# Kernel optimization log

Measured on AMD Instinct MI355X. Metric: run time of the kernel, lower is better.

## Reference

```python
import jax, jax.numpy as jnp
import numpy as np

QMIN, QMAX = -128, 127

def make_accurate_lut():
    # lut[i, j] = signed8(j) * signed8(i) with indices taken as uint8 bit patterns
    v = np.arange(256)
    v[v >= 128] -= 256
    xx, yy = np.meshgrid(v, v)
    return jnp.asarray((xx * yy).astype(np.int32))

def setup_inputs() -> dict:
    key = jax.random.key(0)
    kx, kw = jax.random.split(key)
    B, N, M, K = 4, 512, 512, 256
    x = jax.random.normal(kx, (B, N, M), dtype=jnp.float32)
    w = jax.random.normal(kw, (K, M), dtype=jnp.float32)
    return {
        "x": x,
        "w": w,
        "lut": make_accurate_lut(),                       # [256,256] int32
        "x_scale": jnp.ones((1,), jnp.float32) * 0.03,    # per-tensor affine quant params
        "x_zero_point": jnp.zeros((1,), jnp.float32),
        "w_scale": jnp.ones((1,), jnp.float32) * 0.03,
        "w_zero_point": jnp.zeros((1,), jnp.float32),
    }

def _quantize(t, scale, zp):
    # affine quantize to signed int8 range, kept in int32 for indexing
    q = jnp.round(t / scale + zp)
    return jnp.clip(q, QMIN, QMAX).astype(jnp.int32)

def _lut_gemm(xq, wq, lut):
    # xq: [B,N,M] int32 in [-128,127]; wq: [K,M]; lut: [256,256]
    xi = jnp.mod(xq, 256)  # uint8 bit-pattern index
    wi = jnp.mod(wq, 256)
    # gather per-element products via the LUT, then accumulate over M
    prods = lut[xi[:, :, None, :], wi[None, None, :, :]]  # [B,N,K,M] int32
    return prods.sum(axis=-1)                             # [B,N,K] int32

def reference(x, w, lut, x_scale, x_zero_point, w_scale, w_zero_point):
    xs, xzp = x_scale.reshape(()), x_zero_point.reshape(())
    ws, wzp = w_scale.reshape(()), w_zero_point.reshape(())
    M = x.shape[-1]
    xq = _quantize(x, xs, xzp)           # [B,N,M]
    wq = _quantize(w, ws, wzp)           # [K,M]
    acc = _lut_gemm(xq, wq, lut).astype(jnp.float32)  # ~ sum_m xq*wq via LUT
    # affine zero-point correction: sum (xq-xzp)(wq-wzp)
    acc = (acc
           - wzp * jnp.sum(xq, axis=-1, keepdims=True).astype(jnp.float32)
           - xzp * jnp.sum(wq, axis=-1).astype(jnp.float32)[None, None, :]
           + jnp.float32(M) * xzp * wzp)
    return acc * xs * ws                 # dequantized output [B,N,K]
```

## Files before the change

### kernel.cpp

```cpp
#include <hip/hip_runtime.h>

constexpr int Mdim = 512;
constexpr int Kdim = 256;
constexpr int ROWS = 2048;

typedef int v4i __attribute__((ext_vector_type(4)));

__device__ __forceinline__ int qz(float v, float scale, float zp) {
    float q = rintf(v / scale + zp);
    q = fminf(fmaxf(q, -128.0f), 127.0f);
    return (int)q;
}

__device__ __forceinline__ int qp4(float4 f, float s, float zp) {
    int q0 = qz(f.x, s, zp), q1 = qz(f.y, s, zp);
    int q2 = qz(f.z, s, zp), q3 = qz(f.w, s, zp);
    return (q0 & 255) | ((q1 & 255) << 8) | ((q2 & 255) << 16) | ((q3 & 255) << 24);
}

__global__ __launch_bounds__(64) void fused_lutgemm_kernel(
        const float* __restrict__ x, const float* __restrict__ w,
        const float* __restrict__ x_scale, const float* __restrict__ x_zp,
        const float* __restrict__ w_scale, const float* __restrict__ w_zp,
        float* __restrict__ out) {
    const int lane  = threadIdx.x;
    const int group = lane >> 4;
    const int lo    = lane & 15;
    const int r0 = (blockIdx.x >> 3) * 16;
    const int c0 = (blockIdx.x & 7) * 32;

    const float xs   = x_scale[0], xzpf = x_zp[0];
    const float wsf  = w_scale[0], wzpf = w_zp[0];

    const float4* xr  = (const float4*)(x + (size_t)(r0 + lo) * Mdim) + group * 4;
    const float4* wr0 = (const float4*)(w + (size_t)(c0 + lo) * Mdim) + group * 4;
    const float4* wr1 = (const float4*)(w + (size_t)(c0 + 16 + lo) * Mdim) + group * 4;

    v4i a[8], b0[8], b1[8];
    #pragma unroll
    for (int kk = 0; kk < 8; ++kk) {
        float4 f0 = xr[kk * 16 + 0], f1 = xr[kk * 16 + 1];
        float4 f2 = xr[kk * 16 + 2], f3 = xr[kk * 16 + 3];
        float4 g0 = wr0[kk * 16 + 0], g1 = wr0[kk * 16 + 1];
        float4 g2 = wr0[kk * 16 + 2], g3 = wr0[kk * 16 + 3];
        float4 h0 = wr1[kk * 16 + 0], h1 = wr1[kk * 16 + 1];
        float4 h2 = wr1[kk * 16 + 2], h3 = wr1[kk * 16 + 3];
        a[kk]  = (v4i){ qp4(f0, xs, xzpf),  qp4(f1, xs, xzpf),
                        qp4(f2, xs, xzpf),  qp4(f3, xs, xzpf) };
        b0[kk] = (v4i){ qp4(g0, wsf, wzpf), qp4(g1, wsf, wzpf),
                        qp4(g2, wsf, wzpf), qp4(g3, wsf, wzpf) };
        b1[kk] = (v4i){ qp4(h0, wsf, wzpf), qp4(h1, wsf, wzpf),
                        qp4(h2, wsf, wzpf), qp4(h3, wsf, wzpf) };
    }

    const v4i ones = {0x01010101, 0x01010101, 0x01010101, 0x01010101};
    v4i acc0  = {0, 0, 0, 0};
    v4i acc1  = {0, 0, 0, 0};
    v4i accxs = {0, 0, 0, 0};
    v4i accw0 = {0, 0, 0, 0};
    v4i accw1 = {0, 0, 0, 0};
    #pragma unroll
    for (int kk = 0; kk < 8; ++kk) {
        acc0  = __builtin_amdgcn_mfma_i32_16x16x64_i8(a[kk], b0[kk], acc0, 0, 0, 0);
        acc1  = __builtin_amdgcn_mfma_i32_16x16x64_i8(a[kk], b1[kk], acc1, 0, 0, 0);
        accxs = __builtin_amdgcn_mfma_i32_16x16x64_i8(a[kk], ones,   accxs, 0, 0, 0);
        accw0 = __builtin_amdgcn_mfma_i32_16x16x64_i8(ones,  b0[kk], accw0, 0, 0, 0);
        accw1 = __builtin_amdgcn_mfma_i32_16x16x64_i8(ones,  b1[kk], accw1, 0, 0, 0);
    }

    const float oscale    = xs * wsf;
    const float base_corr = (float)Mdim * xzpf * wzpf;
    const float corr0 = base_corr - xzpf * (float)accw0[0];
    const float corr1 = base_corr - xzpf * (float)accw1[0];

    #pragma unroll
    for (int i = 0; i < 4; ++i) {
        const int row = r0 + group * 4 + i;
        const float xc = wzpf * (float)accxs[i];
        float v0 = (float)acc0[i] - xc + corr0;
        float v1 = (float)acc1[i] - xc + corr1;
        out[(size_t)row * Kdim + c0 + lo]      = v0 * oscale;
        out[(size_t)row * Kdim + c0 + 16 + lo] = v1 * oscale;
    }
}

extern "C" void kernel_launch(void* const* d_in, const int* in_sizes, int n_in,
                              void* d_out, int out_size, void* d_ws, size_t ws_size,
                              hipStream_t stream) {
    const float* x       = (const float*)d_in[0];
    const float* w       = (const float*)d_in[1];
    const float* x_scale = (const float*)d_in[3];
    const float* x_zp    = (const float*)d_in[4];
    const float* w_scale = (const float*)d_in[5];
    const float* w_zp    = (const float*)d_in[6];
    float* out = (float*)d_out;
    (void)d_ws; (void)ws_size;

    fused_lutgemm_kernel<<<(ROWS / 16) * (Kdim / 32), 64, 0, stream>>>(
        x, w, x_scale, x_zp, w_scale, w_zp, out);
}
```

Baseline: 82.11 us.

## Share quantized weight tile across four waves via swizzled LDS

Each block now covers 64 rows with four waves instead of one wave per 16-row tile. The 32x512 weight slice is quantized once per block into XOR-swizzled shared memory and read by all waves, so each block does a quarter of the previous redundant weight loads and quantization. This adds a block-wide barrier and 16KB of LDS per block, and cuts the number of blocks by four, which lowers available parallelism.

```diff
diff --git a/kernel.cpp b/kernel.cpp
--- a/kernel.cpp
+++ b/kernel.cpp
@@ -18,39 +18,59 @@
     return (q0 & 255) | ((q1 & 255) << 8) | ((q2 & 255) << 16) | ((q3 & 255) << 24);
 }
 
-__global__ __launch_bounds__(64) void fused_lutgemm_kernel(
+__global__ __launch_bounds__(256) void fused_lutgemm_kernel(
         const float* __restrict__ x, const float* __restrict__ w,
         const float* __restrict__ x_scale, const float* __restrict__ x_zp,
         const float* __restrict__ w_scale, const float* __restrict__ w_zp,
         float* __restrict__ out) {
-    const int lane  = threadIdx.x;
+    __shared__ int bq[32 * 128];
+
+    const int tid = threadIdx.x;
+    const int r0 = (blockIdx.x >> 3) * 64;
+    const int c0 = (blockIdx.x & 7) * 32;
+
+    const float xs  = x_scale[0], xzpf = x_zp[0];
+    const float wsf = w_scale[0], wzpf = w_zp[0];
+
+    {
+        const int br = tid >> 3;
+        const int g0 = (tid & 7) * 4;
+        const float4* src = (const float4*)(w + (size_t)(c0 + br) * Mdim);
+        #pragma unroll
+        for (int j = 0; j < 4; ++j) {
+            const int g = g0 + j;
+            float4 f0 = src[g * 4 + 0], f1 = src[g * 4 + 1];
+            float4 f2 = src[g * 4 + 2], f3 = src[g * 4 + 3];
+            v4i q = { qp4(f0, wsf, wzpf), qp4(f1, wsf, wzpf),
+                      qp4(f2, wsf, wzpf), qp4(f3, wsf, wzpf) };
+            *(v4i*)&bq[br * 128 + (g ^ (br & 7)) * 4] = q;
+        }
+    }
+
+    const int lane  = tid & 63;
+    const int wv    = tid >> 6;
     const int group = lane >> 4;
     const int lo    = lane & 15;
-    const int r0 = (blockIdx.x >> 3) * 16;
-    const int c0 = (blockIdx.x & 7) * 32;
+    const int arow  = r0 + wv * 16 + lo;
+    const float4* xr = (const float4*)(x + (size_t)arow * Mdim) + group * 4;
 
-    const float xs   = x_scale[0], xzpf = x_zp[0];
-    const float wsf  = w_scale[0], wzpf = w_zp[0];
-
-    const float4* xr  = (const float4*)(x + (size_t)(r0 + lo) * Mdim) + group * 4;
-    const float4* wr0 = (const float4*)(w + (size_t)(c0 + lo) * Mdim) + group * 4;
-    const float4* wr1 = (const float4*)(w + (size_t)(c0 + 16 + lo) * Mdim) + group * 4;
-
-    v4i a[8], b0[8], b1[8];
+    v4i a[8];
     #pragma unroll
     for (int kk = 0; kk < 8; ++kk) {
         float4 f0 = xr[kk * 16 + 0], f1 = xr[kk * 16 + 1];
         float4 f2 = xr[kk * 16 + 2], f3 = xr[kk * 16 + 3];
-        float4 g0 = wr0[kk * 16 + 0], g1 = wr0[kk * 16 + 1];
-        float4 g2 = wr0[kk * 16 + 2], g3 = wr0[kk * 16 + 3];
-        float4 h0 = wr1[kk * 16 + 0], h1 = wr1[kk * 16 + 1];
-        float4 h2 = wr1[kk * 16 + 2], h3 = wr1[kk * 16 + 3];
-        a[kk]  = (v4i){ qp4(f0, xs, xzpf),  qp4(f1, xs, xzpf),
-                        qp4(f2, xs, xzpf),  qp4(f3, xs, xzpf) };
-        b0[kk] = (v4i){ qp4(g0, wsf, wzpf), qp4(g1, wsf, wzpf),
-                        qp4(g2, wsf, wzpf), qp4(g3, wsf, wzpf) };
-        b1[kk] = (v4i){ qp4(h0, wsf, wzpf), qp4(h1, wsf, wzpf),
-                        qp4(h2, wsf, wzpf), qp4(h3, wsf, wzpf) };
+        a[kk] = (v4i){ qp4(f0, xs, xzpf), qp4(f1, xs, xzpf),
+                       qp4(f2, xs, xzpf), qp4(f3, xs, xzpf) };
+    }
+
+    __syncthreads();
+
+    v4i b0[8], b1[8];
+    #pragma unroll
+    for (int kk = 0; kk < 8; ++kk) {
+        const int g = kk * 4 + group;
+        b0[kk] = *(const v4i*)&bq[lo * 128        + (g ^ (lo & 7)) * 4];
+        b1[kk] = *(const v4i*)&bq[(16 + lo) * 128 + (g ^ (lo & 7)) * 4];
     }
 
     const v4i ones = {0x01010101, 0x01010101, 0x01010101, 0x01010101};
@@ -75,7 +95,7 @@
 
     #pragma unroll
     for (int i = 0; i < 4; ++i) {
-        const int row = r0 + group * 4 + i;
+        const int row = r0 + wv * 16 + group * 4 + i;
         const float xc = wzpf * (float)accxs[i];
         float v0 = (float)acc0[i] - xc + corr0;
         float v1 = (float)acc1[i] - xc + corr1;
@@ -96,6 +116,6 @@
     float* out = (float*)d_out;
     (void)d_ws; (void)ws_size;
 
-    fused_lutgemm_kernel<<<(ROWS / 16) * (Kdim / 32), 64, 0, stream>>>(
+    fused_lutgemm_kernel<<<(ROWS / 64) * (Kdim / 32), 256, 0, stream>>>(
         x, w, x_scale, x_zp, w_scale, w_zp, out);
 }
```

Result: faster. 75.92 us (-7.5%).
